# Optimization experiments

Hardware: AMD Instinct MI355X
Metric: run time of the kernel (lower is better)

## Reference

```python
import jax, jax.numpy as jnp
import numpy as np

N = 100000
E = 1600000
F_IN = 128
H = 128
NUM_GRAPHS = 512
EPS = 1e-5


def setup_inputs() -> dict:
    key = jax.random.key(0)
    ks = jax.random.split(key, 16)
    x = jax.random.normal(ks[0], (N, F_IN), dtype=jnp.float32)
    edge_index = jax.random.randint(ks[1], (2, E), 0, N, dtype=jnp.int32)
    batch = jnp.sort(jax.random.randint(ks[2], (N,), 0, NUM_GRAPHS, dtype=jnp.int32))
    def lin(k, fi, fo):
        s = 1.0 / np.sqrt(fi)
        return jax.random.uniform(k, (fi, fo), jnp.float32, -s, s)
    return {
        "x": x, "edge_index": edge_index, "batch": batch,
        "W1": lin(ks[3], F_IN, H), "b1": jnp.zeros((H,), jnp.float32),
        "g1": jnp.ones((H,), jnp.float32), "beta1": jnp.zeros((H,), jnp.float32),
        "W2": lin(ks[4], H, H), "b2": jnp.zeros((H,), jnp.float32),
        "g2": jnp.ones((H,), jnp.float32), "beta2": jnp.zeros((H,), jnp.float32),
        "W3": lin(ks[5], H, H), "b3": jnp.zeros((H,), jnp.float32),
        "g3": jnp.ones((H,), jnp.float32), "beta3": jnp.zeros((H,), jnp.float32),
        "Wl": lin(ks[6], H, 1), "bl": jnp.zeros((1,), jnp.float32),
    }


def _layer_norm(x, g, b):
    mu = jnp.mean(x, axis=-1, keepdims=True)
    var = jnp.mean((x - mu) ** 2, axis=-1, keepdims=True)
    return (x - mu) * jax.lax.rsqrt(var + EPS) * g + b


def _gcn_conv(x, W, b, src, dst, dinv):
    # GCNConv: D^{-1/2}(A+I)D^{-1/2} X W + b, deg includes self-loops
    h = x @ W                                   # [N,H]
    enorm = dinv[src] * dinv[dst]               # [E]
    agg = jax.ops.segment_sum(h[src] * enorm[:, None], dst, num_segments=N)
    agg = agg + h * (dinv * dinv)[:, None]      # self-loop contribution
    return agg + b


def reference(x, edge_index, batch, W1, b1, g1, beta1, W2, b2, g2, beta2,
              W3, b3, g3, beta3, Wl, bl):
    src, dst = edge_index[0], edge_index[1]
    deg = 1.0 + jax.ops.segment_sum(jnp.ones((E,), jnp.float32), dst, num_segments=N)
    dinv = jax.lax.rsqrt(deg)
    h = jax.nn.relu(_layer_norm(_gcn_conv(x, W1, b1, src, dst, dinv), g1, beta1))
    h = jax.nn.relu(_layer_norm(_gcn_conv(h, W2, b2, src, dst, dinv), g2, beta2))
    h = jax.nn.relu(_layer_norm(_gcn_conv(h, W3, b3, src, dst, dinv), g3, beta3))
    # global mean pool over graphs
    sums = jax.ops.segment_sum(h, batch, num_segments=NUM_GRAPHS)
    cnts = jax.ops.segment_sum(jnp.ones((N,), jnp.float32), batch, num_segments=NUM_GRAPHS)
    pooled = sums / jnp.maximum(cnts, 1.0)[:, None]
    return pooled @ Wl + bl                     # [NUM_GRAPHS, 1]
```

## Files before the change

### kernel.cpp

```cpp
#include <hip/hip_runtime.h>
#include <hip/hip_bf16.h>
#include <math.h>

#define N_NODES    100000
#define N_EDGES    1600000
#define FDIM       128
#define NUM_GRAPHS 512
#define EPS        1e-5f
#define PADN       100096

#define B_CVT   12512
#define B_WPK   192

#define NBUCK   196
#define CAPA    9216
#define EB_CHUNK 2048
#define BIN_BLOCKS ((N_EDGES + EB_CHUNK - 1) / EB_CHUNK)
#define SEGSH   14
#define SEGN    8

typedef __attribute__((ext_vector_type(8))) __bf16 bf16x8;
typedef __attribute__((ext_vector_type(4))) float  f32x4;

__device__ __forceinline__ unsigned short f2bf(float f) {
    unsigned u = __builtin_bit_cast(unsigned, f);
    u += 0x7FFF + ((u >> 16) & 1);
    return (unsigned short)(u >> 16);
}
__device__ __forceinline__ float bf2f(unsigned short b) {
    unsigned u = ((unsigned)b) << 16;
    return __builtin_bit_cast(float, u);
}

__device__ __forceinline__ void dec4(unsigned dw, float* o) {
    auto lo = __builtin_amdgcn_cvt_pk_f32_fp8(dw, false);
    auto hi = __builtin_amdgcn_cvt_pk_f32_fp8(dw, true);
    o[0] = lo[0]; o[1] = lo[1]; o[2] = hi[0]; o[3] = hi[1];
}

__device__ __forceinline__ void acc16(uint4 v, float* a) {
    float d[16];
    dec4(v.x, &d[0]); dec4(v.y, &d[4]); dec4(v.z, &d[8]); dec4(v.w, &d[12]);
#pragma unroll
    for (int f = 0; f < 16; f++) a[f] += d[f];
}

__device__ __forceinline__ void agg_core(const unsigned char* __restrict__ h8,
                                         const int* __restrict__ offs,
                                         const int* __restrict__ csr_src,
                                         float di, int i, int sl,
                                         const float* __restrict__ bias,
                                         const float* __restrict__ gamma,
                                         const float* __restrict__ beta,
                                         unsigned* ow) {
    size_t lofs16 = (size_t)sl * 16;
    float a[16];
    {
        uint4 v = *(const uint4*)(h8 + (size_t)i * 128 + lofs16);
        float d[16];
        dec4(v.x, &d[0]); dec4(v.y, &d[4]); dec4(v.z, &d[8]); dec4(v.w, &d[12]);
#pragma unroll
        for (int f = 0; f < 16; f++) a[f] = d[f];
    }

    int eBeg = offs[i], eEnd = offs[i + 1];
    int e = eBeg;
    int s0, s1, s2, s3;
    if (e + 4 <= eEnd) {
        s0 = csr_src[e + 0]; s1 = csr_src[e + 1];
        s2 = csr_src[e + 2]; s3 = csr_src[e + 3];
    }
    for (; e + 8 <= eEnd; e += 4) {
        uint4 v0 = *(const uint4*)(h8 + (size_t)s0 * 128 + lofs16);
        uint4 v1 = *(const uint4*)(h8 + (size_t)s1 * 128 + lofs16);
        uint4 v2 = *(const uint4*)(h8 + (size_t)s2 * 128 + lofs16);
        uint4 v3 = *(const uint4*)(h8 + (size_t)s3 * 128 + lofs16);
        s0 = csr_src[e + 4]; s1 = csr_src[e + 5];
        s2 = csr_src[e + 6]; s3 = csr_src[e + 7];
        acc16(v0, a); acc16(v1, a); acc16(v2, a); acc16(v3, a);
    }
    if (e + 4 <= eEnd) {
        uint4 v0 = *(const uint4*)(h8 + (size_t)s0 * 128 + lofs16);
        uint4 v1 = *(const uint4*)(h8 + (size_t)s1 * 128 + lofs16);
        uint4 v2 = *(const uint4*)(h8 + (size_t)s2 * 128 + lofs16);
        uint4 v3 = *(const uint4*)(h8 + (size_t)s3 * 128 + lofs16);
        acc16(v0, a); acc16(v1, a); acc16(v2, a); acc16(v3, a);
        e += 4;
    }
    for (; e < eEnd; ++e) {
        int s = csr_src[e];
        uint4 v = *(const uint4*)(h8 + (size_t)s * 128 + lofs16);
        acc16(v, a);
    }

    float4 b0 = *(const float4*)(bias + sl * 16);
    float4 b1 = *(const float4*)(bias + sl * 16 + 4);
    float4 b2 = *(const float4*)(bias + sl * 16 + 8);
    float4 b3 = *(const float4*)(bias + sl * 16 + 12);
    a[0]  = fmaf(a[0],  di, b0.x); a[1]  = fmaf(a[1],  di, b0.y);
    a[2]  = fmaf(a[2],  di, b0.z); a[3]  = fmaf(a[3],  di, b0.w);
    a[4]  = fmaf(a[4],  di, b1.x); a[5]  = fmaf(a[5],  di, b1.y);
    a[6]  = fmaf(a[6],  di, b1.z); a[7]  = fmaf(a[7],  di, b1.w);
    a[8]  = fmaf(a[8],  di, b2.x); a[9]  = fmaf(a[9],  di, b2.y);
    a[10] = fmaf(a[10], di, b2.z); a[11] = fmaf(a[11], di, b2.w);
    a[12] = fmaf(a[12], di, b3.x); a[13] = fmaf(a[13], di, b3.y);
    a[14] = fmaf(a[14], di, b3.z); a[15] = fmaf(a[15], di, b3.w);

    float s1v = 0.f, s2v = 0.f;
#pragma unroll
    for (int f = 0; f < 16; f++) { s1v += a[f]; s2v += a[f] * a[f]; }
#pragma unroll
    for (int off = 1; off < 8; off <<= 1) {
        s1v += __shfl_xor(s1v, off);
        s2v += __shfl_xor(s2v, off);
    }
    float mu   = s1v * (1.0f / 128.0f);
    float var  = s2v * (1.0f / 128.0f) - mu * mu;
    float rstd = rsqrtf(var + EPS);

    float4 g0 = *(const float4*)(gamma + sl * 16);
    float4 g1 = *(const float4*)(gamma + sl * 16 + 4);
    float4 g2 = *(const float4*)(gamma + sl * 16 + 8);
    float4 g3 = *(const float4*)(gamma + sl * 16 + 12);
    float4 e0v = *(const float4*)(beta + sl * 16);
    float4 e1v = *(const float4*)(beta + sl * 16 + 4);
    float4 e2v = *(const float4*)(beta + sl * 16 + 8);
    float4 e3v = *(const float4*)(beta + sl * 16 + 12);
    float g[16]  = {g0.x,g0.y,g0.z,g0.w, g1.x,g1.y,g1.z,g1.w,
                    g2.x,g2.y,g2.z,g2.w, g3.x,g3.y,g3.z,g3.w};
    float be[16] = {e0v.x,e0v.y,e0v.z,e0v.w, e1v.x,e1v.y,e1v.z,e1v.w,
                    e2v.x,e2v.y,e2v.z,e2v.w, e3v.x,e3v.y,e3v.z,e3v.w};

#pragma unroll
    for (int f = 0; f < 8; f++) {
        float r0 = fmaxf((a[2*f]   - mu) * rstd * g[2*f]   + be[2*f],   0.f);
        float r1 = fmaxf((a[2*f+1] - mu) * rstd * g[2*f+1] + be[2*f+1], 0.f);
        ow[f] = (unsigned)f2bf(r0) | ((unsigned)f2bf(r1) << 16);
    }
}


__global__ __launch_bounds__(256) void k_bin(const int* __restrict__ src,
                                             const int* __restrict__ dst,
                                             int* __restrict__ bcur,
                                             unsigned* __restrict__ binned) {
    __shared__ int hist[NBUCK];
    __shared__ int lbase[NBUCK];
    __shared__ int loff[NBUCK];
    __shared__ unsigned lpack[EB_CHUNK];
    __shared__ unsigned short lbuck[EB_CHUNK];
    int b = blockIdx.x;
    int t = threadIdx.x;
    int e0 = b * EB_CHUNK;
    int nE = min(EB_CHUNK, N_EDGES - e0);

    for (int j = t; j < NBUCK; j += 256) { hist[j] = 0; loff[j] = 0; }
    __syncthreads();

    for (int k = t; k < nE; k += 256) {
        int e  = e0 + k;
        int d  = dst[e];
        int bk = d >> 9;
        lpack[k] = (unsigned)src[e] | ((unsigned)(d & 511) << 17);
        lbuck[k] = (unsigned short)bk;
        atomicAdd(&hist[bk], 1);
    }
    __syncthreads();
    for (int j = t; j < NBUCK; j += 256)
        lbase[j] = atomicAdd(&bcur[j], hist[j]);
    __syncthreads();

    for (int k = t; k < nE; k += 256) {
        int bk = lbuck[k];
        int p  = lbase[bk] + atomicAdd(&loff[bk], 1);
        binned[(size_t)bk * CAPA + p] = lpack[k];
    }
}


__global__ __launch_bounds__(256) void k_mid(const unsigned* __restrict__ binned,
                                             const int* __restrict__ bcur,
                                             int* __restrict__ offs,
                                             float* __restrict__ dinv,
                                             int* __restrict__ csr_src,
                                             const float* __restrict__ x,
                                             unsigned short* __restrict__ xb,
                                             const float* __restrict__ W1,
                                             const float* __restrict__ W2,
                                             const float* __restrict__ W3,
                                             unsigned short* __restrict__ wp) {
    __shared__ int smem[512 * SEGN + 256];
    int b = blockIdx.x;
    int t = threadIdx.x;

    if (b < NBUCK) {
        int* cnt2 = smem;
        int* part = smem + 4096;
        int nb0 = b * 512;
        int cnt = bcur[b];

        int pv = (t < b) ? bcur[t] : 0;
#pragma unroll
        for (int off = 32; off; off >>= 1) pv += __shfl_down(pv, off);
        if ((t & 63) == 0) part[t >> 6] = pv;
        __syncthreads();
        int seg0 = part[0] + part[1] + part[2] + part[3];
        __syncthreads();

        for (int j = t; j < 512 * SEGN; j += 256) cnt2[j] = 0;
        __syncthreads();

        for (int k = t; k < cnt; k += 256) {
            unsigned v = binned[(size_t)b * CAPA + k];
            atomicAdd(&cnt2[(v >> 17) * SEGN + ((v & 0x1FFFF) >> SEGSH)], 1);
        }
        __syncthreads();

        int base16 = t * 16;
        int lsum[16];
        int run = 0;
#pragma unroll
        for (int q = 0; q < 16; q++) { lsum[q] = run; run += cnt2[base16 + q]; }
        int deg0 = lsum[8];
        int deg1 = run - lsum[8];
        part[t] = run;
        __syncthreads();
        for (int off = 1; off < 256; off <<= 1) {
            int y = 0;
            if (t >= off) y = part[t - off];
            __syncthreads();
            if (t >= off) part[t] += y;
            __syncthreads();
        }
        int excl = part[t] - run;
#pragma unroll
        for (int q = 0; q < 16; q++) cnt2[base16 + q] = excl + lsum[q];

        {
            int n0 = nb0 + 2 * t;
            if (n0 < N_NODES) {
                offs[n0] = seg0 + excl;
                dinv[n0] = rsqrtf(1.0f + (float)deg0);
            }
            if (n0 + 1 < N_NODES) {
                offs[n0 + 1] = seg0 + excl + lsum[8];
                dinv[n0 + 1] = rsqrtf(1.0f + (float)deg1);
            }
        }
        if (b == NBUCK - 1 && t == 0) offs[N_NODES] = N_EDGES;
        __syncthreads();

        for (int k = t; k < cnt; k += 256) {
            unsigned v = binned[(size_t)b * CAPA + k];
            int p = atomicAdd(&cnt2[(v >> 17) * SEGN + ((v & 0x1FFFF) >> SEGSH)], 1);
            csr_src[seg0 + p] = (int)(v & 0x1FFFF);
        }
    } else if (b < NBUCK + B_CVT) {
        long long idx = ((long long)(b - NBUCK) * 256 + t) * 4;
        ushort4 o;
        if (idx < (long long)N_NODES * FDIM) {
            float4 v = *(const float4*)(x + idx);
            o.x = f2bf(v.x); o.y = f2bf(v.y); o.z = f2bf(v.z); o.w = f2bf(v.w);
        } else {
            o.x = o.y = o.z = o.w = 0;
        }
        *(ushort4*)(xb + idx) = o;
    } else {
        int wb  = b - (NBUCK + B_CVT);
        int mat = wb >> 6;
        const float* W = (mat == 0) ? W1 : (mat == 1) ? W2 : W3;
        unsigned short* o = wp + (size_t)mat * 16384;
        int idx = (wb & 63) * 256 + t;
        int j  = idx & 7;
        int l  = (idx >> 3) & 63;
        int ct = (idx >> 9) & 7;
        int ks = idx >> 12;
        int k  = ks * 32 + (l >> 4) * 8 + j;
        int c  = ct * 16 + (l & 15);
        o[idx] = f2bf(W[k * 128 + c]);
    }
}


__global__ __launch_bounds__(256) void k_gemm(const unsigned short* __restrict__ A,
                                              const unsigned short* __restrict__ Wp,
                                              const float* __restrict__ dinv,
                                              unsigned char* __restrict__ C8) {
    int t    = threadIdx.x;
    int lane = t & 63;
    int w    = t >> 6;
    int wc   = w & 1;
    int wr   = w >> 1;
    int rb   = blockIdx.x * 128 + wr * 64 + (lane & 15);
    int koff = (lane >> 4) * 8;

    f32x4 acc[4][4];
#pragma unroll
    for (int c = 0; c < 4; c++)
#pragma unroll
        for (int r = 0; r < 4; r++) acc[c][r] = (f32x4){0.f, 0.f, 0.f, 0.f};

    const bf16x8* Wv = (const bf16x8*)Wp;
#pragma unroll
    for (int ks = 0; ks < 4; ++ks) {
        bf16x8 fw[4], fa[4];
#pragma unroll
        for (int c = 0; c < 4; ++c)
            fw[c] = Wv[(ks * 8 + wc * 4 + c) * 64 + lane];
#pragma unroll
        for (int r = 0; r < 4; ++r) {
            const uint4 v = *(const uint4*)(A + (size_t)(rb + r * 16) * 128 + ks * 32 + koff);
            fa[r] = __builtin_bit_cast(bf16x8, v);
        }
#pragma unroll
        for (int c = 0; c < 4; ++c)
#pragma unroll
            for (int r = 0; r < 4; ++r)
                acc[c][r] = __builtin_amdgcn_mfma_f32_16x16x32_bf16(fw[c], fa[r], acc[c][r], 0, 0, 0);
    }

#pragma unroll
    for (int r = 0; r < 4; ++r) {
        int row = blockIdx.x * 128 + wr * 64 + r * 16 + (lane & 15);
        if (row < N_NODES) {
            float dv = dinv[row];
#pragma unroll
            for (int c = 0; c < 4; ++c) {
                int col = (wc * 4 + c) * 16 + (lane >> 4) * 4;
                unsigned u = __builtin_amdgcn_cvt_pk_fp8_f32(acc[c][r][0] * dv, acc[c][r][1] * dv, 0, false);
                u = (unsigned)__builtin_amdgcn_cvt_pk_fp8_f32(acc[c][r][2] * dv, acc[c][r][3] * dv, (int)u, true);
                *(unsigned*)(C8 + (size_t)row * 128 + col) = u;
            }
        }
    }
}


__global__ __launch_bounds__(256, 4) void k_fused(const unsigned char* __restrict__ h8_in,
                                                  const unsigned short* __restrict__ Wp,
                                                  const float* __restrict__ dinv,
                                                  unsigned char* __restrict__ h8_out,
                                                  const int* __restrict__ offs,
                                                  const int* __restrict__ csr_src,
                                                  const float* __restrict__ bias,
                                                  const float* __restrict__ gamma,
                                                  const float* __restrict__ beta) {
    __shared__ unsigned tile_u[128 * 64];
    int t    = threadIdx.x;
    int lane = t & 63;
    int w    = t >> 6;
    int grp  = lane >> 3;
    int sl   = lane & 7;
    int r0   = blockIdx.x * 128;

    for (int pass = 0; pass < 4; ++pass) {
        int nt = pass * 32 + w * 8 + grp;
        int i  = r0 + nt;
        unsigned ow[8];
        if (i < N_NODES) {
            agg_core(h8_in, offs, csr_src, dinv[i], i, sl, bias, gamma, beta, ow);
        } else {
#pragma unroll
            for (int f = 0; f < 8; f++) ow[f] = 0;
        }
        int rowbase = nt * 64;
        int colu    = sl * 8;
        int swz0 = (colu    ) ^ ((nt & 15) << 2);
        int swz1 = (colu + 4) ^ ((nt & 15) << 2);
        *(uint4*)&tile_u[rowbase + swz0] = make_uint4(ow[0], ow[1], ow[2], ow[3]);
        *(uint4*)&tile_u[rowbase + swz1] = make_uint4(ow[4], ow[5], ow[6], ow[7]);
    }
    __syncthreads();

    int wc = w & 1;
    int wr = w >> 1;
    f32x4 acc[4][4];
#pragma unroll
    for (int c = 0; c < 4; c++)
#pragma unroll
        for (int r = 0; r < 4; r++) acc[c][r] = (f32x4){0.f, 0.f, 0.f, 0.f};

    const bf16x8* Wv = (const bf16x8*)Wp;
#pragma unroll
    for (int ks = 0; ks < 4; ++ks) {
        bf16x8 fw[4], fa[4];
#pragma unroll
        for (int c = 0; c < 4; ++c)
            fw[c] = Wv[(ks * 8 + wc * 4 + c) * 64 + lane];
#pragma unroll
        for (int r = 0; r < 4; ++r) {
            int lr   = wr * 64 + r * 16 + (lane & 15);
            int colu = ks * 16 + (lane >> 4) * 4;
            int swz  = colu ^ ((lr & 15) << 2);
            uint4 v = *(const uint4*)&tile_u[lr * 64 + swz];
            fa[r] = __builtin_bit_cast(bf16x8, v);
        }
#pragma unroll
        for (int c = 0; c < 4; ++c)
#pragma unroll
            for (int r = 0; r < 4; ++r)
                acc[c][r] = __builtin_amdgcn_mfma_f32_16x16x32_bf16(fw[c], fa[r], acc[c][r], 0, 0, 0);
    }

#pragma unroll
    for (int r = 0; r < 4; ++r) {
        int row = r0 + wr * 64 + r * 16 + (lane & 15);
        if (row < N_NODES) {
            float dv = dinv[row];
#pragma unroll
            for (int c = 0; c < 4; ++c) {
                int col = (wc * 4 + c) * 16 + (lane >> 4) * 4;
                unsigned u = __builtin_amdgcn_cvt_pk_fp8_f32(acc[c][r][0] * dv, acc[c][r][1] * dv, 0, false);
                u = (unsigned)__builtin_amdgcn_cvt_pk_fp8_f32(acc[c][r][2] * dv, acc[c][r][3] * dv, (int)u, true);
                *(unsigned*)(h8_out + (size_t)row * 128 + col) = u;
            }
        }
    }
}


__global__ __launch_bounds__(256) void k_agg(const unsigned char* __restrict__ h8,
                                             unsigned short* __restrict__ out,
                                             const int* __restrict__ offs,
                                             const int* __restrict__ csr_src,
                                             const float* __restrict__ dinv,
                                             const float* __restrict__ bias,
                                             const float* __restrict__ gamma,
                                             const float* __restrict__ beta) {
    int t    = threadIdx.x;
    int lane = t & 63;
    int grp  = lane >> 3;
    int sl   = lane & 7;
    int i    = blockIdx.x * 32 + (t >> 6) * 8 + grp;

    unsigned ow[8];
    agg_core(h8, offs, csr_src, dinv[i], i, sl, bias, gamma, beta, ow);

    uint4* op = (uint4*)(out + (size_t)i * 128 + sl * 16);
    op[0] = make_uint4(ow[0], ow[1], ow[2], ow[3]);
    op[1] = make_uint4(ow[4], ow[5], ow[6], ow[7]);
}


__global__ __launch_bounds__(256) void k_pool(const unsigned short* __restrict__ h,
                                              const int* __restrict__ batch,
                                              const float* __restrict__ Wl,
                                              const float* __restrict__ bl,
                                              float* __restrict__ out) {
    __shared__ float2 part[4][64];
    int g = blockIdx.x;
    int t = threadIdx.x, w = t >> 6, lane = t & 63;

    int lo = 0, hi = N_NODES;
    while (lo < hi) { int mid = (lo + hi) >> 1; if (batch[mid] < g) lo = mid + 1; else hi = mid; }
    int s = lo;
    lo = s; hi = N_NODES;
    while (lo < hi) { int mid = (lo + hi) >> 1; if (batch[mid] < g + 1) lo = mid + 1; else hi = mid; }
    int e = lo;

    float ax = 0.f, ay = 0.f;
    for (int n = s + w; n < e; n += 4) {
        unsigned v = *(const unsigned*)(h + (size_t)n * 128 + lane * 2);
        ax += bf2f((unsigned short)(v & 0xffff));
        ay += bf2f((unsigned short)(v >> 16));
    }
    part[w][lane] = make_float2(ax, ay);
    __syncthreads();
    if (t < 64) {
        float sx = part[0][lane].x + part[1][lane].x + part[2][lane].x + part[3][lane].x;
        float sy = part[0][lane].y + part[1][lane].y + part[2][lane].y + part[3][lane].y;
        float cnt = fmaxf((float)(e - s), 1.0f);
        float inv = 1.0f / cnt;
        float p = sx * inv * Wl[lane * 2] + sy * inv * Wl[lane * 2 + 1];
#pragma unroll
        for (int off = 32; off; off >>= 1) p += __shfl_xor(p, off);
        if (lane == 0) out[g] = p + bl[0];
    }
}


extern "C" void kernel_launch(void* const* d_in, const int* in_sizes, int n_in,
                              void* d_out, int out_size, void* d_ws, size_t ws_size,
                              hipStream_t stream) {
    const float* x     = (const float*)d_in[0];
    const int*   ei    = (const int*)d_in[1];
    const int*   batch = (const int*)d_in[2];
    const float* W1 = (const float*)d_in[3];
    const float* b1 = (const float*)d_in[4];
    const float* g1 = (const float*)d_in[5];
    const float* be1 = (const float*)d_in[6];
    const float* W2 = (const float*)d_in[7];
    const float* b2 = (const float*)d_in[8];
    const float* g2 = (const float*)d_in[9];
    const float* be2 = (const float*)d_in[10];
    const float* W3 = (const float*)d_in[11];
    const float* b3 = (const float*)d_in[12];
    const float* g3 = (const float*)d_in[13];
    const float* be3 = (const float*)d_in[14];
    const float* Wl = (const float*)d_in[15];
    const float* bl = (const float*)d_in[16];

    const int* src = ei;
    const int* dst = ei + N_EDGES;

    char* ws = (char*)d_ws;
    size_t off = 0;
    auto alloc = [&](size_t bytes) -> void* {
        void* p = ws + off;
        off += (bytes + 255) & ~(size_t)255;
        return p;
    };
    unsigned short* xb   = (unsigned short*)alloc((size_t)PADN * FDIM * 2);
    unsigned short* hA   = (unsigned short*)alloc((size_t)PADN * FDIM * 2);
    unsigned char*  hFa  = (unsigned char*)alloc((size_t)PADN * FDIM);
    unsigned char*  hFb  = (unsigned char*)alloc((size_t)PADN * FDIM);
    unsigned short* wp   = (unsigned short*)alloc((size_t)3 * 16384 * 2);
    float* dinv    = (float*)alloc((size_t)N_NODES * 4);
    int*   offs    = (int*)alloc((size_t)(N_NODES + 1) * 4);
    int*   csr_src = (int*)alloc((size_t)N_EDGES * 4);
    unsigned* binned = (unsigned*)alloc((size_t)NBUCK * CAPA * 4);
    int*   bcur    = (int*)alloc(256 * 4);

    hipMemsetAsync(bcur, 0, 256 * 4, stream);

    k_bin<<<BIN_BLOCKS, 256, 0, stream>>>(src, dst, bcur, binned);
    k_mid<<<NBUCK + B_CVT + B_WPK, 256, 0, stream>>>(binned, bcur, offs, dinv, csr_src,
                                                     x, xb, W1, W2, W3, wp);

    int gemm_grid  = PADN / 128;
    int agg_grid   = N_NODES / 32;

    k_gemm<<<gemm_grid, 256, 0, stream>>>(xb, wp, dinv, hFa);
    k_fused<<<gemm_grid, 256, 0, stream>>>(hFa, wp + 16384, dinv, hFb,
                                           offs, csr_src, b1, g1, be1);
    k_fused<<<gemm_grid, 256, 0, stream>>>(hFb, wp + 32768, dinv, hFa,
                                           offs, csr_src, b2, g2, be2);
    k_agg<<<agg_grid, 256, 0, stream>>>(hFa, hA, offs, csr_src, dinv, b3, g3, be3);

    k_pool<<<NUM_GRAPHS, 256, 0, stream>>>(hA, batch, Wl, bl, (float*)d_out);
}
```

Measured before the change: 244.2 us.

## Fuse final aggregation with mean pooling, shrink fused tiles, regroup preprocessing kernels

The last aggregation layer now accumulates per-graph sums directly into a pooled buffer with atomics, so the bf16 hidden-state write and the separate pool kernel's reread go away. A small final kernel applies the mean and the linear head. The fused aggregate+GEMM kernel now handles 32 rows per block instead of 128, giving more blocks and a smaller LDS tile at the cost of reloading W fragments more often. Edge binning is merged with the x/W conversion kernel, and CSR build becomes its own kernel, which moves the conversion work off the CSR critical path.

```diff
diff --git a/kernel.cpp b/kernel.cpp
--- a/kernel.cpp
+++ b/kernel.cpp
@@ -45,14 +45,14 @@
     for (int f = 0; f < 16; f++) a[f] += d[f];
 }
 
-__device__ __forceinline__ void agg_core(const unsigned char* __restrict__ h8,
-                                         const int* __restrict__ offs,
-                                         const int* __restrict__ csr_src,
-                                         float di, int i, int sl,
-                                         const float* __restrict__ bias,
-                                         const float* __restrict__ gamma,
-                                         const float* __restrict__ beta,
-                                         unsigned* ow) {
+__device__ __forceinline__ void agg_core_f(const unsigned char* __restrict__ h8,
+                                           const int* __restrict__ offs,
+                                           const int* __restrict__ csr_src,
+                                           float di, int i, int sl,
+                                           const float* __restrict__ bias,
+                                           const float* __restrict__ gamma,
+                                           const float* __restrict__ beta,
+                                           float* r) {
     size_t lofs16 = (size_t)sl * 16;
     float a[16];
     {
@@ -132,18 +132,21 @@
                     e2v.x,e2v.y,e2v.z,e2v.w, e3v.x,e3v.y,e3v.z,e3v.w};
 
 #pragma unroll
-    for (int f = 0; f < 8; f++) {
-        float r0 = fmaxf((a[2*f]   - mu) * rstd * g[2*f]   + be[2*f],   0.f);
-        float r1 = fmaxf((a[2*f+1] - mu) * rstd * g[2*f+1] + be[2*f+1], 0.f);
-        ow[f] = (unsigned)f2bf(r0) | ((unsigned)f2bf(r1) << 16);
-    }
-}
-
-
-__global__ __launch_bounds__(256) void k_bin(const int* __restrict__ src,
+    for (int f = 0; f < 16; f++)
+        r[f] = fmaxf((a[f] - mu) * rstd * g[f] + be[f], 0.f);
+}
+
+
+__global__ __launch_bounds__(256) void k_pre(const int* __restrict__ src,
                                              const int* __restrict__ dst,
                                              int* __restrict__ bcur,
-                                             unsigned* __restrict__ binned) {
+                                             unsigned* __restrict__ binned,
+                                             const float* __restrict__ x,
+                                             unsigned short* __restrict__ xb,
+                                             const float* __restrict__ W1,
+                                             const float* __restrict__ W2,
+                                             const float* __restrict__ W3,
+                                             unsigned short* __restrict__ wp) {
     __shared__ int hist[NBUCK];
     __shared__ int lbase[NBUCK];
     __shared__ int loff[NBUCK];
@@ -151,112 +154,33 @@
     __shared__ unsigned short lbuck[EB_CHUNK];
     int b = blockIdx.x;
     int t = threadIdx.x;
-    int e0 = b * EB_CHUNK;
-    int nE = min(EB_CHUNK, N_EDGES - e0);
-
-    for (int j = t; j < NBUCK; j += 256) { hist[j] = 0; loff[j] = 0; }
-    __syncthreads();
-
-    for (int k = t; k < nE; k += 256) {
-        int e  = e0 + k;
-        int d  = dst[e];
-        int bk = d >> 9;
-        lpack[k] = (unsigned)src[e] | ((unsigned)(d & 511) << 17);
-        lbuck[k] = (unsigned short)bk;
-        atomicAdd(&hist[bk], 1);
-    }
-    __syncthreads();
-    for (int j = t; j < NBUCK; j += 256)
-        lbase[j] = atomicAdd(&bcur[j], hist[j]);
-    __syncthreads();
-
-    for (int k = t; k < nE; k += 256) {
-        int bk = lbuck[k];
-        int p  = lbase[bk] + atomicAdd(&loff[bk], 1);
-        binned[(size_t)bk * CAPA + p] = lpack[k];
-    }
-}
-
-
-__global__ __launch_bounds__(256) void k_mid(const unsigned* __restrict__ binned,
-                                             const int* __restrict__ bcur,
-                                             int* __restrict__ offs,
-                                             float* __restrict__ dinv,
-                                             int* __restrict__ csr_src,
-                                             const float* __restrict__ x,
-                                             unsigned short* __restrict__ xb,
-                                             const float* __restrict__ W1,
-                                             const float* __restrict__ W2,
-                                             const float* __restrict__ W3,
-                                             unsigned short* __restrict__ wp) {
-    __shared__ int smem[512 * SEGN + 256];
-    int b = blockIdx.x;
-    int t = threadIdx.x;
-
-    if (b < NBUCK) {
-        int* cnt2 = smem;
-        int* part = smem + 4096;
-        int nb0 = b * 512;
-        int cnt = bcur[b];
-
-        int pv = (t < b) ? bcur[t] : 0;
-#pragma unroll
-        for (int off = 32; off; off >>= 1) pv += __shfl_down(pv, off);
-        if ((t & 63) == 0) part[t >> 6] = pv;
-        __syncthreads();
-        int seg0 = part[0] + part[1] + part[2] + part[3];
-        __syncthreads();
-
-        for (int j = t; j < 512 * SEGN; j += 256) cnt2[j] = 0;
-        __syncthreads();
-
-        for (int k = t; k < cnt; k += 256) {
-            unsigned v = binned[(size_t)b * CAPA + k];
-            atomicAdd(&cnt2[(v >> 17) * SEGN + ((v & 0x1FFFF) >> SEGSH)], 1);
-        }
-        __syncthreads();
-
-        int base16 = t * 16;
-        int lsum[16];
-        int run = 0;
-#pragma unroll
-        for (int q = 0; q < 16; q++) { lsum[q] = run; run += cnt2[base16 + q]; }
-        int deg0 = lsum[8];
-        int deg1 = run - lsum[8];
-        part[t] = run;
-        __syncthreads();
-        for (int off = 1; off < 256; off <<= 1) {
-            int y = 0;
-            if (t >= off) y = part[t - off];
-            __syncthreads();
-            if (t >= off) part[t] += y;
-            __syncthreads();
-        }
-        int excl = part[t] - run;
-#pragma unroll
-        for (int q = 0; q < 16; q++) cnt2[base16 + q] = excl + lsum[q];
-
-        {
-            int n0 = nb0 + 2 * t;
-            if (n0 < N_NODES) {
-                offs[n0] = seg0 + excl;
-                dinv[n0] = rsqrtf(1.0f + (float)deg0);
-            }
-            if (n0 + 1 < N_NODES) {
-                offs[n0 + 1] = seg0 + excl + lsum[8];
-                dinv[n0 + 1] = rsqrtf(1.0f + (float)deg1);
-            }
-        }
-        if (b == NBUCK - 1 && t == 0) offs[N_NODES] = N_EDGES;
-        __syncthreads();
-
-        for (int k = t; k < cnt; k += 256) {
-            unsigned v = binned[(size_t)b * CAPA + k];
-            int p = atomicAdd(&cnt2[(v >> 17) * SEGN + ((v & 0x1FFFF) >> SEGSH)], 1);
-            csr_src[seg0 + p] = (int)(v & 0x1FFFF);
-        }
-    } else if (b < NBUCK + B_CVT) {
-        long long idx = ((long long)(b - NBUCK) * 256 + t) * 4;
+    if (b < BIN_BLOCKS) {
+        int e0 = b * EB_CHUNK;
+        int nE = min(EB_CHUNK, N_EDGES - e0);
+
+        for (int j = t; j < NBUCK; j += 256) { hist[j] = 0; loff[j] = 0; }
+        __syncthreads();
+
+        for (int k = t; k < nE; k += 256) {
+            int e  = e0 + k;
+            int d  = dst[e];
+            int bk = d >> 9;
+            lpack[k] = (unsigned)src[e] | ((unsigned)(d & 511) << 17);
+            lbuck[k] = (unsigned short)bk;
+            atomicAdd(&hist[bk], 1);
+        }
+        __syncthreads();
+        for (int j = t; j < NBUCK; j += 256)
+            lbase[j] = atomicAdd(&bcur[j], hist[j]);
+        __syncthreads();
+
+        for (int k = t; k < nE; k += 256) {
+            int bk = lbuck[k];
+            int p  = lbase[bk] + atomicAdd(&loff[bk], 1);
+            binned[(size_t)bk * CAPA + p] = lpack[k];
+        }
+    } else if (b < BIN_BLOCKS + B_CVT) {
+        long long idx = ((long long)(b - BIN_BLOCKS) * 256 + t) * 4;
         ushort4 o;
         if (idx < (long long)N_NODES * FDIM) {
             float4 v = *(const float4*)(x + idx);
@@ -266,7 +190,7 @@
         }
         *(ushort4*)(xb + idx) = o;
     } else {
-        int wb  = b - (NBUCK + B_CVT);
+        int wb  = b - (BIN_BLOCKS + B_CVT);
         int mat = wb >> 6;
         const float* W = (mat == 0) ? W1 : (mat == 1) ? W2 : W3;
         unsigned short* o = wp + (size_t)mat * 16384;
@@ -282,6 +206,78 @@
 }
 
 
+__global__ __launch_bounds__(256) void k_binB(const unsigned* __restrict__ binned,
+                                              const int* __restrict__ bcur,
+                                              int* __restrict__ offs,
+                                              float* __restrict__ dinv,
+                                              int* __restrict__ csr_src) {
+    __shared__ int smem[512 * SEGN + 256];
+    int* cnt2 = smem;
+    int* part = smem + 4096;
+    int b = blockIdx.x;
+    int t = threadIdx.x;
+    int nb0 = b * 512;
+    int cnt = bcur[b];
+
+    int pv = (t < b) ? bcur[t] : 0;
+#pragma unroll
+    for (int off = 32; off; off >>= 1) pv += __shfl_down(pv, off);
+    if ((t & 63) == 0) part[t >> 6] = pv;
+    __syncthreads();
+    int seg0 = part[0] + part[1] + part[2] + part[3];
+    __syncthreads();
+
+    for (int j = t; j < 512 * SEGN; j += 256) cnt2[j] = 0;
+    __syncthreads();
+
+    for (int k = t; k < cnt; k += 256) {
+        unsigned v = binned[(size_t)b * CAPA + k];
+        atomicAdd(&cnt2[(v >> 17) * SEGN + ((v & 0x1FFFF) >> SEGSH)], 1);
+    }
+    __syncthreads();
+
+    int base16 = t * 16;
+    int lsum[16];
+    int run = 0;
+#pragma unroll
+    for (int q = 0; q < 16; q++) { lsum[q] = run; run += cnt2[base16 + q]; }
+    int deg0 = lsum[8];
+    int deg1 = run - lsum[8];
+    part[t] = run;
+    __syncthreads();
+    for (int off = 1; off < 256; off <<= 1) {
+        int y = 0;
+        if (t >= off) y = part[t - off];
+        __syncthreads();
+        if (t >= off) part[t] += y;
+        __syncthreads();
+    }
+    int excl = part[t] - run;
+#pragma unroll
+    for (int q = 0; q < 16; q++) cnt2[base16 + q] = excl + lsum[q];
+
+    {
+        int n0 = nb0 + 2 * t;
+        if (n0 < N_NODES) {
+            offs[n0] = seg0 + excl;
+            dinv[n0] = rsqrtf(1.0f + (float)deg0);
+        }
+        if (n0 + 1 < N_NODES) {
+            offs[n0 + 1] = seg0 + excl + lsum[8];
+            dinv[n0 + 1] = rsqrtf(1.0f + (float)deg1);
+        }
+    }
+    if (b == NBUCK - 1 && t == 0) offs[N_NODES] = N_EDGES;
+    __syncthreads();
+
+    for (int k = t; k < cnt; k += 256) {
+        unsigned v = binned[(size_t)b * CAPA + k];
+        int p = atomicAdd(&cnt2[(v >> 17) * SEGN + ((v & 0x1FFFF) >> SEGSH)], 1);
+        csr_src[seg0 + p] = (int)(v & 0x1FFFF);
+    }
+}
+
+
 __global__ __launch_bounds__(256) void k_gemm(const unsigned short* __restrict__ A,
                                               const unsigned short* __restrict__ Wp,
                                               const float* __restrict__ dinv,
@@ -345,24 +341,22 @@
                                                   const float* __restrict__ bias,
                                                   const float* __restrict__ gamma,
                                                   const float* __restrict__ beta) {
-    __shared__ unsigned tile_u[128 * 64];
+    __shared__ unsigned tile_u[32 * 64];
     int t    = threadIdx.x;
     int lane = t & 63;
     int w    = t >> 6;
     int grp  = lane >> 3;
     int sl   = lane & 7;
-    int r0   = blockIdx.x * 128;
-
-    for (int pass = 0; pass < 4; ++pass) {
-        int nt = pass * 32 + w * 8 + grp;
-        int i  = r0 + nt;
+    int nt   = w * 8 + grp;
+    int i    = blockIdx.x * 32 + nt;
+
+    {
+        float r[16];
+        agg_core_f(h8_in, offs, csr_src, dinv[i], i, sl, bias, gamma, beta, r);
         unsigned ow[8];
-        if (i < N_NODES) {
-            agg_core(h8_in, offs, csr_src, dinv[i], i, sl, bias, gamma, beta, ow);
-        } else {
-#pragma unroll
-            for (int f = 0; f < 8; f++) ow[f] = 0;
-        }
+#pragma unroll
+        for (int f = 0; f < 8; f++)
+            ow[f] = (unsigned)f2bf(r[2 * f]) | ((unsigned)f2bf(r[2 * f + 1]) << 16);
         int rowbase = nt * 64;
         int colu    = sl * 8;
         int swz0 = (colu    ) ^ ((nt & 15) << 2);
@@ -372,84 +366,110 @@
     }
     __syncthreads();
 
-    int wc = w & 1;
-    int wr = w >> 1;
-    f32x4 acc[4][4];
-#pragma unroll
-    for (int c = 0; c < 4; c++)
-#pragma unroll
-        for (int r = 0; r < 4; r++) acc[c][r] = (f32x4){0.f, 0.f, 0.f, 0.f};
+    f32x4 acc[2][2];
+#pragma unroll
+    for (int c = 0; c < 2; c++)
+#pragma unroll
+        for (int r = 0; r < 2; r++) acc[c][r] = (f32x4){0.f, 0.f, 0.f, 0.f};
 
     const bf16x8* Wv = (const bf16x8*)Wp;
 #pragma unroll
     for (int ks = 0; ks < 4; ++ks) {
-        bf16x8 fw[4], fa[4];
-#pragma unroll
-        for (int c = 0; c < 4; ++c)
-            fw[c] = Wv[(ks * 8 + wc * 4 + c) * 64 + lane];
-#pragma unroll
-        for (int r = 0; r < 4; ++r) {
-            int lr   = wr * 64 + r * 16 + (lane & 15);
+        bf16x8 fw[2], fa[2];
+#pragma unroll
+        for (int c = 0; c < 2; ++c)
+            fw[c] = Wv[(ks * 8 + w * 2 + c) * 64 + lane];
+#pragma unroll
+        for (int r = 0; r < 2; ++r) {
+            int lr   = r * 16 + (lane & 15);
             int colu = ks * 16 + (lane >> 4) * 4;
             int swz  = colu ^ ((lr & 15) << 2);
             uint4 v = *(const uint4*)&tile_u[lr * 64 + swz];
             fa[r] = __builtin_bit_cast(bf16x8, v);
         }
 #pragma unroll
-        for (int c = 0; c < 4; ++c)
-#pragma unroll
-            for (int r = 0; r < 4; ++r)
+        for (int c = 0; c < 2; ++c)
+#pragma unroll
+            for (int r = 0; r < 2; ++r)
                 acc[c][r] = __builtin_amdgcn_mfma_f32_16x16x32_bf16(fw[c], fa[r], acc[c][r], 0, 0, 0);
     }
 
 #pragma unroll
-    for (int r = 0; r < 4; ++r) {
-        int row = r0 + wr * 64 + r * 16 + (lane & 15);
-        if (row < N_NODES) {
-            float dv = dinv[row];
-#pragma unroll
-            for (int c = 0; c < 4; ++c) {
-                int col = (wc * 4 + c) * 16 + (lane >> 4) * 4;
-                unsigned u = __builtin_amdgcn_cvt_pk_fp8_f32(acc[c][r][0] * dv, acc[c][r][1] * dv, 0, false);
-                u = (unsigned)__builtin_amdgcn_cvt_pk_fp8_f32(acc[c][r][2] * dv, acc[c][r][3] * dv, (int)u, true);
-                *(unsigned*)(h8_out + (size_t)row * 128 + col) = u;
-            }
-        }
-    }
-}
-
-
-__global__ __launch_bounds__(256) void k_agg(const unsigned char* __restrict__ h8,
-                                             unsigned short* __restrict__ out,
-                                             const int* __restrict__ offs,
-                                             const int* __restrict__ csr_src,
-                                             const float* __restrict__ dinv,
-                                             const float* __restrict__ bias,
-                                             const float* __restrict__ gamma,
-                                             const float* __restrict__ beta) {
+    for (int r = 0; r < 2; ++r) {
+        int row = blockIdx.x * 32 + r * 16 + (lane & 15);
+        float dv = dinv[row];
+#pragma unroll
+        for (int c = 0; c < 2; ++c) {
+            int col = (w * 2 + c) * 16 + (lane >> 4) * 4;
+            unsigned u = __builtin_amdgcn_cvt_pk_fp8_f32(acc[c][r][0] * dv, acc[c][r][1] * dv, 0, false);
+            u = (unsigned)__builtin_amdgcn_cvt_pk_fp8_f32(acc[c][r][2] * dv, acc[c][r][3] * dv, (int)u, true);
+            *(unsigned*)(h8_out + (size_t)row * 128 + col) = u;
+        }
+    }
+}
+
+
+__global__ __launch_bounds__(256) void k_aggpool(const unsigned char* __restrict__ h8,
+                                                 const int* __restrict__ offs,
+                                                 const int* __restrict__ csr_src,
+                                                 const float* __restrict__ dinv,
+                                                 const int* __restrict__ batch,
+                                                 const float* __restrict__ bias,
+                                                 const float* __restrict__ gamma,
+                                                 const float* __restrict__ beta,
+                                                 float* __restrict__ pooled) {
+    __shared__ float wsum[4][128];
+    __shared__ int grange[2];
     int t    = threadIdx.x;
     int lane = t & 63;
+    int w    = t >> 6;
     int grp  = lane >> 3;
     int sl   = lane & 7;
-    int i    = blockIdx.x * 32 + (t >> 6) * 8 + grp;
-
-    unsigned ow[8];
-    agg_core(h8, offs, csr_src, dinv[i], i, sl, bias, gamma, beta, ow);
-
-    uint4* op = (uint4*)(out + (size_t)i * 128 + sl * 16);
-    op[0] = make_uint4(ow[0], ow[1], ow[2], ow[3]);
-    op[1] = make_uint4(ow[4], ow[5], ow[6], ow[7]);
-}
-
-
-__global__ __launch_bounds__(256) void k_pool(const unsigned short* __restrict__ h,
+    int i    = blockIdx.x * 32 + w * 8 + grp;
+
+    float r[16];
+    agg_core_f(h8, offs, csr_src, dinv[i], i, sl, bias, gamma, beta, r);
+
+    int bg = batch[i];
+    if (t == 0) {
+        grange[0] = batch[blockIdx.x * 32];
+        grange[1] = batch[blockIdx.x * 32 + 31];
+    }
+    __syncthreads();
+    int g0 = grange[0], g1 = grange[1];
+
+    for (int g = g0; g <= g1; ++g) {
+        float v[16];
+        bool in = (bg == g);
+#pragma unroll
+        for (int f = 0; f < 16; f++) v[f] = in ? r[f] : 0.f;
+#pragma unroll
+        for (int f = 0; f < 16; f++) {
+            v[f] += __shfl_xor(v[f], 8);
+            v[f] += __shfl_xor(v[f], 16);
+            v[f] += __shfl_xor(v[f], 32);
+        }
+        if (grp == 0) {
+#pragma unroll
+            for (int f = 0; f < 16; f++) wsum[w][sl * 16 + f] = v[f];
+        }
+        __syncthreads();
+        if (t < 128) {
+            float s = wsum[0][t] + wsum[1][t] + wsum[2][t] + wsum[3][t];
+            if (s != 0.f) atomicAdd(&pooled[(size_t)g * 128 + t], s);
+        }
+        __syncthreads();
+    }
+}
+
+
+__global__ __launch_bounds__(64) void k_final(const float* __restrict__ pooled,
                                               const int* __restrict__ batch,
                                               const float* __restrict__ Wl,
                                               const float* __restrict__ bl,
                                               float* __restrict__ out) {
-    __shared__ float2 part[4][64];
     int g = blockIdx.x;
-    int t = threadIdx.x, w = t >> 6, lane = t & 63;
+    int lane = threadIdx.x;
 
     int lo = 0, hi = N_NODES;
     while (lo < hi) { int mid = (lo + hi) >> 1; if (batch[mid] < g) lo = mid + 1; else hi = mid; }
@@ -458,24 +478,12 @@
     while (lo < hi) { int mid = (lo + hi) >> 1; if (batch[mid] < g + 1) lo = mid + 1; else hi = mid; }
     int e = lo;
 
-    float ax = 0.f, ay = 0.f;
-    for (int n = s + w; n < e; n += 4) {
-        unsigned v = *(const unsigned*)(h + (size_t)n * 128 + lane * 2);
-        ax += bf2f((unsigned short)(v & 0xffff));
-        ay += bf2f((unsigned short)(v >> 16));
-    }
-    part[w][lane] = make_float2(ax, ay);
-    __syncthreads();
-    if (t < 64) {
-        float sx = part[0][lane].x + part[1][lane].x + part[2][lane].x + part[3][lane].x;
-        float sy = part[0][lane].y + part[1][lane].y + part[2][lane].y + part[3][lane].y;
-        float cnt = fmaxf((float)(e - s), 1.0f);
-        float inv = 1.0f / cnt;
-        float p = sx * inv * Wl[lane * 2] + sy * inv * Wl[lane * 2 + 1];
-#pragma unroll
-        for (int off = 32; off; off >>= 1) p += __shfl_xor(p, off);
-        if (lane == 0) out[g] = p + bl[0];
-    }
+    float inv = 1.0f / fmaxf((float)(e - s), 1.0f);
+    float2 p2 = ((const float2*)(pooled + (size_t)g * 128))[lane];
+    float p = p2.x * inv * Wl[lane * 2] + p2.y * inv * Wl[lane * 2 + 1];
+#pragma unroll
+    for (int off = 32; off; off >>= 1) p += __shfl_xor(p, off);
+    if (lane == 0) out[g] = p + bl[0];
 }
 
 
@@ -511,7 +519,6 @@
         return p;
     };
     unsigned short* xb   = (unsigned short*)alloc((size_t)PADN * FDIM * 2);
-    unsigned short* hA   = (unsigned short*)alloc((size_t)PADN * FDIM * 2);
     unsigned char*  hFa  = (unsigned char*)alloc((size_t)PADN * FDIM);
     unsigned char*  hFb  = (unsigned char*)alloc((size_t)PADN * FDIM);
     unsigned short* wp   = (unsigned short*)alloc((size_t)3 * 16384 * 2);
@@ -520,22 +527,24 @@
     int*   csr_src = (int*)alloc((size_t)N_EDGES * 4);
     unsigned* binned = (unsigned*)alloc((size_t)NBUCK * CAPA * 4);
     int*   bcur    = (int*)alloc(256 * 4);
+    float* pooled  = (float*)alloc((size_t)NUM_GRAPHS * FDIM * 4);
 
     hipMemsetAsync(bcur, 0, 256 * 4, stream);
-
-    k_bin<<<BIN_BLOCKS, 256, 0, stream>>>(src, dst, bcur, binned);
-    k_mid<<<NBUCK + B_CVT + B_WPK, 256, 0, stream>>>(binned, bcur, offs, dinv, csr_src,
-                                                     x, xb, W1, W2, W3, wp);
+    hipMemsetAsync(pooled, 0, (size_t)NUM_GRAPHS * FDIM * 4, stream);
+
+    k_pre<<<BIN_BLOCKS + B_CVT + B_WPK, 256, 0, stream>>>(src, dst, bcur, binned,
+                                                          x, xb, W1, W2, W3, wp);
+    k_binB<<<NBUCK, 256, 0, stream>>>(binned, bcur, offs, dinv, csr_src);
 
     int gemm_grid  = PADN / 128;
-    int agg_grid   = N_NODES / 32;
+    int fuse_grid  = N_NODES / 32;
 
     k_gemm<<<gemm_grid, 256, 0, stream>>>(xb, wp, dinv, hFa);
-    k_fused<<<gemm_grid, 256, 0, stream>>>(hFa, wp + 16384, dinv, hFb,
+    k_fused<<<fuse_grid, 256, 0, stream>>>(hFa, wp + 16384, dinv, hFb,
                                            offs, csr_src, b1, g1, be1);
-    k_fused<<<gemm_grid, 256, 0, stream>>>(hFb, wp + 32768, dinv, hFa,
+    k_fused<<<fuse_grid, 256, 0, stream>>>(hFb, wp + 32768, dinv, hFa,
                                            offs, csr_src, b2, g2, be2);
-    k_agg<<<agg_grid, 256, 0, stream>>>(hFa, hA, offs, csr_src, dinv, b3, g3, be3);
-
-    k_pool<<<NUM_GRAPHS, 256, 0, stream>>>(hA, batch, Wl, bl, (float*)d_out);
-}
+    k_aggpool<<<fuse_grid, 256, 0, stream>>>(hFa, offs, csr_src, dinv, batch,
+                                             b3, g3, be3, pooled);
+    k_final<<<NUM_GRAPHS, 64, 0, stream>>>(pooled, batch, Wl, bl, (float*)d_out);
+}
```

New measurement: 234.5 us. 1.04x faster.
